# Kernel tuning notes

Hardware: AMD Instinct MI355X
Metric: run time of the kernel (lower is better)

Reference implementation:

```python
import jax, jax.numpy as jnp
import numpy as np

B, NLB, NPB, SDIM = 128, 32, 160, 256  # complexes, ligand atoms, pocket CAs, scalar dim


def _uniform(key, shape, fan_in):
    # kaiming_uniform_(a=sqrt(5)) -> U(-1/sqrt(fan_in), 1/sqrt(fan_in))
    bound = 1.0 / np.sqrt(fan_in)
    return jax.random.uniform(key, shape, jnp.float32, -bound, bound)


def setup_inputs() -> dict:
    key = jax.random.key(0)
    k1, k2, k3, k4, k5 = jax.random.split(key, 5)
    NL, NP = B * NLB, B * NPB
    # block-diagonal cross adjacency: every ligand atom paired with every pocket CA
    # of the same complex (same as (batch_ligand[:,None]==batch_pocket[None,:]).nonzero().T)
    l = np.repeat(np.arange(NL, dtype=np.int32), NPB)
    p = (np.arange(B, dtype=np.int32)[:, None, None] * NPB
         + np.zeros((1, NLB, 1), dtype=np.int32)
         + np.arange(NPB, dtype=np.int32)[None, None, :]).reshape(-1)
    return {
        "s_ligand": jax.random.normal(k1, (NL, SDIM), jnp.float32),
        "s_pocket": jax.random.normal(k2, (NP, SDIM), jnp.float32),
        "l": jnp.asarray(l),
        "p": jnp.asarray(p),
        "W1": _uniform(k3, (SDIM // 2, SDIM), SDIM),
        "b1": jnp.zeros((SDIM // 2,), jnp.float32),
        "W2": _uniform(k4, (SDIM // 4, SDIM // 2), SDIM // 2),
        "b2": jnp.zeros((SDIM // 4,), jnp.float32),
        "W3": _uniform(k5, (1, SDIM // 4), SDIM // 4),
        "b3": jnp.zeros((1,), jnp.float32),
    }


def reference(s_ligand, s_pocket, l, p, W1, b1, W2, b2, W3, b3):
    # gather cross-pair embeddings and sum: s[e] = s_ligand[l[e]] + s_pocket[p[e]]
    s = s_ligand[l] + s_pocket[p]                      # [E, sdim]
    h = jax.nn.silu(s @ W1.T + b1)                     # [E, sdim/2]
    h = jax.nn.silu(h @ W2.T + b2)                     # [E, sdim/4]
    out = jax.nn.relu(h @ W3.T + b3)                   # [E, 1]
    return out.squeeze(-1)                             # [E]
```

## Files before the change

kernel.cpp:

```cpp
#include <hip/hip_runtime.h>
#include <hip/hip_bf16.h>


#define B_CPLX   128
#define NLB      32
#define NPB      160
#define SDIM     256
#define H1DIM    128
#define NL_TOT   (B_CPLX * NLB)
#define NP_TOT   (B_CPLX * NPB)
#define NROWS    (NL_TOT + NP_TOT)
#define E_TOT    (B_CPLX * NLB * NPB)

#define W1_LDS_STRIDE 264
#define JT_CHUNK 16
#define ZP_STRIDE 132

#define EDGE_BLOCKS (B_CPLX * 10)

#define NEG_LOG2E -1.4426950408889634f
#define NEG_LN2   -0.69314718055994531f

typedef __bf16 bf16x8 __attribute__((ext_vector_type(8)));
typedef __bf16 bf16x2 __attribute__((ext_vector_type(2)));
typedef unsigned short ushortx8 __attribute__((ext_vector_type(8)));
typedef unsigned short ushortx4 __attribute__((ext_vector_type(4)));
typedef unsigned uintx4 __attribute__((ext_vector_type(4)));
typedef float f32x4 __attribute__((ext_vector_type(4)));
typedef float f32x2 __attribute__((ext_vector_type(2)));

#if __has_builtin(__builtin_amdgcn_exp2f)
#define EXP2F(x) __builtin_amdgcn_exp2f(x)
#else
#define EXP2F(x) exp2f(x)
#endif

__device__ __forceinline__ unsigned short f2bf(float f) {
    unsigned u = __builtin_bit_cast(unsigned, f);
    u += 0x7FFFu + ((u >> 16) & 1u);
    return (unsigned short)(u >> 16);
}

__device__ __forceinline__ unsigned perm_hi16u(unsigned u0, unsigned u1) {
    return __builtin_amdgcn_perm(u1, u0, 0x07060302u);
}

__device__ __forceinline__ unsigned pack2_rhu(float x0, float x1) {
    unsigned u0 = __builtin_bit_cast(unsigned, x0) + 0x8000u;
    unsigned u1 = __builtin_bit_cast(unsigned, x1) + 0x8000u;
    return perm_hi16u(u0, u1);
}

__device__ __forceinline__ bf16x8 pack8_rne(const float* x) {
    bf16x8 r;
#pragma unroll
    for (int j = 0; j < 4; ++j) {
        f32x2 p = {x[2 * j], x[2 * j + 1]};
        bf16x2 b = __builtin_convertvector(p, bf16x2);
        r[2 * j]     = b[0];
        r[2 * j + 1] = b[1];
    }
    return r;
}

__device__ __forceinline__ void pack_split(const float* x, bf16x8& hi, bf16x8& lo) {
    uintx4 h, l;
#pragma unroll
    for (int j = 0; j < 4; ++j) {
        float x0 = x[2 * j], x1 = x[2 * j + 1];
        unsigned u0 = __builtin_bit_cast(unsigned, x0);
        unsigned u1 = __builtin_bit_cast(unsigned, x1);
        h[j] = perm_hi16u(u0, u1);
        float hf0 = __builtin_bit_cast(float, u0 & 0xFFFF0000u);
        float hf1 = __builtin_bit_cast(float, u1 & 0xFFFF0000u);
        l[j] = pack2_rhu(x0 - hf0, x1 - hf1);
    }
    hi = __builtin_bit_cast(bf16x8, h);
    lo = __builtin_bit_cast(bf16x8, l);
}

__device__ __forceinline__ float silu_u(float t) {
    float e = EXP2F(t);
    float r = __builtin_amdgcn_rcpf(1.0f + e);
    return t * r;
}

__device__ __forceinline__ float rowsum16(float s) {
    int b;
    b = __builtin_bit_cast(int, s);
    b = __builtin_amdgcn_update_dpp(b, b, 0x121, 0xF, 0xF, false);
    s += __builtin_bit_cast(float, b);
    b = __builtin_bit_cast(int, s);
    b = __builtin_amdgcn_update_dpp(b, b, 0x122, 0xF, 0xF, false);
    s += __builtin_bit_cast(float, b);
    b = __builtin_bit_cast(int, s);
    b = __builtin_amdgcn_update_dpp(b, b, 0x124, 0xF, 0xF, false);
    s += __builtin_bit_cast(float, b);
    b = __builtin_bit_cast(int, s);
    b = __builtin_amdgcn_update_dpp(b, b, 0x128, 0xF, 0xF, false);
    s += __builtin_bit_cast(float, b);
    return s;
}

__global__ __launch_bounds__(256) void proj_kernel(
    const float* __restrict__ s_lig, const float* __restrict__ s_poc,
    const float* __restrict__ W1,    const float* __restrict__ b1,
    float* __restrict__ Z)
{
    __shared__ unsigned short w1s[64 * W1_LDS_STRIDE];

    const int tid  = threadIdx.x;
    const int tg   = blockIdx.x >> 1;
    const int half = blockIdx.x & 1;

    {
        const f32x4* w4 = (const f32x4*)(W1 + (size_t)half * 64 * SDIM);
#pragma unroll
        for (int r = 0; r < 2; ++r) {
            f32x4 t[8];
#pragma unroll
            for (int s = 0; s < 8; ++s) t[s] = w4[tid + (r * 8 + s) * 256];
#pragma unroll
            for (int s = 0; s < 8; ++s) {
                const int u = tid + (r * 8 + s) * 256;
                const int n = u >> 6;
                const int k4 = u & 63;
                ushortx4 us;
#pragma unroll
                for (int j = 0; j < 4; ++j) us[j] = f2bf(t[s][j]);
                *(ushortx4*)(&w1s[n * W1_LDS_STRIDE + k4 * 4]) = us;
            }
        }
    }
    __syncthreads();

    const int lane = tid & 63;
    const int widx = tid >> 6;
    const int c    = lane & 15;
    const int q    = lane >> 4;
    const int tile = tg * 4 + widx;
    const int row  = tile * 16 + c;

    const float* src = (row < NL_TOT) ? (s_lig + (size_t)row * SDIM)
                                      : (s_poc + (size_t)(row - NL_TOT) * SDIM);

    f32x4 acc[4];
#pragma unroll
    for (int nt = 0; nt < 4; ++nt) acc[nt] = (f32x4){0.f, 0.f, 0.f, 0.f};

#pragma unroll
    for (int ks = 0; ks < 8; ++ks) {
        const int k0 = ks * 32 + q * 8;
        f32x4 xa = *reinterpret_cast<const f32x4*>(src + k0);
        f32x4 xb = *reinterpret_cast<const f32x4*>(src + k0 + 4);
        float xv[8] = {xa[0], xa[1], xa[2], xa[3], xb[0], xb[1], xb[2], xb[3]};
        bf16x8 ahi, alo;
        pack_split(xv, ahi, alo);
        bf16x8 bfrag[4];
#pragma unroll
        for (int nt = 0; nt < 4; ++nt)
            bfrag[nt] = *reinterpret_cast<const bf16x8*>(
                &w1s[(nt * 16 + c) * W1_LDS_STRIDE + k0]);
#pragma unroll
        for (int nt = 0; nt < 4; ++nt)
            acc[nt] = __builtin_amdgcn_mfma_f32_16x16x32_bf16(ahi, bfrag[nt], acc[nt], 0, 0, 0);
#pragma unroll
        for (int nt = 0; nt < 4; ++nt)
            acc[nt] = __builtin_amdgcn_mfma_f32_16x16x32_bf16(alo, bfrag[nt], acc[nt], 0, 0, 0);
    }

    const int mb = tile * 16 + q * 4;
#pragma unroll
    for (int nt = 0; nt < 4; ++nt) {
        const int n = half * 64 + nt * 16 + c;
        const float bias = b1[n];
#pragma unroll
        for (int r = 0; r < 4; ++r) {
            const int m = mb + r;
            float v = acc[nt][r];
            if (m < NL_TOT) v += bias;
            Z[(size_t)m * H1DIM + n] = v;
        }
    }
}

__global__ __launch_bounds__(256) void edge_kernel(
    const float* __restrict__ Z,
    const float* __restrict__ W2, const float* __restrict__ b2,
    const float* __restrict__ W3, const float* __restrict__ b3,
    float* __restrict__ out)
{
    __shared__ float zp[JT_CHUNK * ZP_STRIDE];
    __shared__ float zl[NLB * H1DIM];
    __shared__ unsigned short w2s[16 * 64 * 8];

    const int tid = threadIdx.x;
    const int b   = blockIdx.x / 10;
    const int jt  = blockIdx.x - b * 10;

    {
#pragma unroll
        for (int s = 0; s < 4; ++s) {
            const int slot   = tid + s * 256;
            const int lane_s = slot & 63;
            const int chunk  = slot >> 6;
            const int nt     = chunk >> 2;
            const int ks     = chunk & 3;
            const int n      = nt * 16 + (lane_s & 15);
            const int k0     = ks * 32 + (lane_s >> 4) * 8;
            const float* wsrc = W2 + (size_t)n * H1DIM + k0;
            f32x4 wa = *(const f32x4*)wsrc;
            f32x4 wb = *(const f32x4*)(wsrc + 4);
            ushortx8 us;
#pragma unroll
            for (int j = 0; j < 4; ++j) {
                us[j]     = f2bf(wa[j]);
                us[4 + j] = f2bf(wb[j]);
            }
            *(ushortx8*)(&w2s[slot * 8]) = us;
        }
    }

    {
        const float* zpg = Z + (size_t)(NL_TOT + b * NPB + jt * JT_CHUNK) * H1DIM;
#pragma unroll
        for (int s = 0; s < 2; ++s) {
            const int u   = tid + s * 256;
            const int row = u >> 5;
            const int c4  = u & 31;
            f32x4 v = *(const f32x4*)(zpg + (size_t)row * H1DIM + c4 * 4);
            v *= NEG_LOG2E;
            *(f32x4*)(&zp[row * ZP_STRIDE + c4 * 4]) = v;
        }
    }

    {
        const float* zlg = Z + (size_t)(b * NLB) * H1DIM;
#pragma unroll
        for (int s = 0; s < 4; ++s) {
            const int u   = tid + s * 256;
            const int row = u >> 5;
            const int c4  = u & 31;
            f32x4 v = *(const f32x4*)(zlg + (size_t)row * H1DIM + c4 * 4);
            v *= NEG_LOG2E;
            *(f32x4*)(&zl[row * H1DIM + c4 * 4]) = v;
        }
    }

    const int lane = tid & 63;
    const int widx = tid >> 6;
    const int c    = lane & 15;
    const int q    = lane >> 4;

    float b2f[4], w3f[4];
#pragma unroll
    for (int nt = 0; nt < 4; ++nt) {
        b2f[nt] = b2[nt * 16 + c] * NEG_LOG2E;
        w3f[nt] = W3[nt * 16 + c] * NEG_LN2;
    }
    const float b3v = b3[0];

    __syncthreads();

    const float* prow = &zp[c * ZP_STRIDE];
    const unsigned short* wbase = &w2s[lane * 8];

#pragma unroll
    for (int h = 0; h < 2; ++h) {
        f32x4 acc[4][4];
#pragma unroll
        for (int a = 0; a < 4; ++a)
#pragma unroll
            for (int nt = 0; nt < 4; ++nt) {
                const float bb = b2f[nt];
                acc[a][nt] = (f32x4){bb, bb, bb, bb};
            }

        const float* lrow0 = &zl[(h * 16 + widx * 4) * H1DIM];

#pragma unroll
        for (int ks = 0; ks < 4; ++ks) {
            const int k0 = ks * 32 + q * 8;
            bf16x8 bfr[4];
#pragma unroll
            for (int nt = 0; nt < 4; ++nt)
                bfr[nt] = *(const bf16x8*)(wbase + (nt * 4 + ks) * 512);
            f32x4 pa = *(const f32x4*)(prow + k0);
            f32x4 pb = *(const f32x4*)(prow + k0 + 4);
#pragma unroll
            for (int a = 0; a < 4; ++a) {
                f32x4 la0 = *(const f32x4*)(lrow0 + a * H1DIM + k0);
                f32x4 la1 = *(const f32x4*)(lrow0 + a * H1DIM + k0 + 4);
                float hv[8];
#pragma unroll
                for (int j = 0; j < 4; ++j) {
                    hv[j]     = silu_u(pa[j] + la0[j]);
                    hv[4 + j] = silu_u(pb[j] + la1[j]);
                }
                bf16x8 af = pack8_rne(hv);
#pragma unroll
                for (int nt = 0; nt < 4; ++nt)
                    acc[a][nt] = __builtin_amdgcn_mfma_f32_16x16x32_bf16(af, bfr[nt], acc[a][nt], 0, 0, 0);
            }
        }

#pragma unroll
        for (int at = 0; at < 4; ++at) {
            const f32x4* A = acc[at];
            float s0 = 0.f, s1 = 0.f, s2 = 0.f, s3 = 0.f;
#pragma unroll
            for (int nt = 0; nt < 4; ++nt) {
                s0 += silu_u(A[nt][0]) * w3f[nt];
                s1 += silu_u(A[nt][1]) * w3f[nt];
                s2 += silu_u(A[nt][2]) * w3f[nt];
                s3 += silu_u(A[nt][3]) * w3f[nt];
            }
            s0 = rowsum16(s0);
            s1 = rowsum16(s1);
            s2 = rowsum16(s2);
            s3 = rowsum16(s3);
            if (c < 4) {
                float v = (c == 0) ? s0 : (c == 1) ? s1 : (c == 2) ? s2 : s3;
                const int e0 = (b * NLB + h * 16 + widx * 4 + at) * NPB + jt * JT_CHUNK;
                out[e0 + q * 4 + c] = fmaxf(v + b3v, 0.0f);
            }
        }
    }
}

extern "C" void kernel_launch(void* const* d_in, const int* in_sizes, int n_in,
                              void* d_out, int out_size, void* d_ws, size_t ws_size,
                              hipStream_t stream)
{
    const float* s_lig = (const float*)d_in[0];
    const float* s_poc = (const float*)d_in[1];
    const float* W1    = (const float*)d_in[4];
    const float* b1    = (const float*)d_in[5];
    const float* W2    = (const float*)d_in[6];
    const float* b2    = (const float*)d_in[7];
    const float* W3    = (const float*)d_in[8];
    const float* b3    = (const float*)d_in[9];

    float* Z = (float*)d_ws;

    hipLaunchKernelGGL(proj_kernel, dim3(NROWS / 16 / 4 * 2), dim3(256), 0, stream,
                       s_lig, s_poc, W1, b1, Z);
    hipLaunchKernelGGL(edge_kernel, dim3(EDGE_BLOCKS), dim3(256), 0, stream,
                       Z, W2, b2, W3, b3, (float*)d_out);
}
```

Before: 131.4 us.

## Prepack W2 in proj kernel, fold exp scaling into W1, swap MFMA operands

Block 0 of the projection kernel now converts W2 to bf16 fragment layout once and stores it in workspace, so edge blocks copy it directly instead of converting per block. The -log2(e) scale is folded into W1 and b1, which removes the per-element multiply when Z is staged in the edge kernel. The layer-2 MFMA operands are swapped so each lane holds four output channels for one edge, letting the W3 dot product finish with two cross-lane shuffles instead of four 16-lane DPP row sums. The cost is an extra workspace buffer and a small serial W2 conversion inside one proj block.

```diff
diff --git a/kernel.cpp b/kernel.cpp
--- a/kernel.cpp
+++ b/kernel.cpp
@@ -85,27 +85,11 @@
     return t * r;
 }
 
-__device__ __forceinline__ float rowsum16(float s) {
-    int b;
-    b = __builtin_bit_cast(int, s);
-    b = __builtin_amdgcn_update_dpp(b, b, 0x121, 0xF, 0xF, false);
-    s += __builtin_bit_cast(float, b);
-    b = __builtin_bit_cast(int, s);
-    b = __builtin_amdgcn_update_dpp(b, b, 0x122, 0xF, 0xF, false);
-    s += __builtin_bit_cast(float, b);
-    b = __builtin_bit_cast(int, s);
-    b = __builtin_amdgcn_update_dpp(b, b, 0x124, 0xF, 0xF, false);
-    s += __builtin_bit_cast(float, b);
-    b = __builtin_bit_cast(int, s);
-    b = __builtin_amdgcn_update_dpp(b, b, 0x128, 0xF, 0xF, false);
-    s += __builtin_bit_cast(float, b);
-    return s;
-}
-
 __global__ __launch_bounds__(256) void proj_kernel(
     const float* __restrict__ s_lig, const float* __restrict__ s_poc,
     const float* __restrict__ W1,    const float* __restrict__ b1,
-    float* __restrict__ Z)
+    const float* __restrict__ W2,
+    float* __restrict__ Z,           unsigned short* __restrict__ W2F)
 {
     __shared__ unsigned short w1s[64 * W1_LDS_STRIDE];
 
@@ -113,92 +97,7 @@
     const int tg   = blockIdx.x >> 1;
     const int half = blockIdx.x & 1;
 
-    {
-        const f32x4* w4 = (const f32x4*)(W1 + (size_t)half * 64 * SDIM);
-#pragma unroll
-        for (int r = 0; r < 2; ++r) {
-            f32x4 t[8];
-#pragma unroll
-            for (int s = 0; s < 8; ++s) t[s] = w4[tid + (r * 8 + s) * 256];
-#pragma unroll
-            for (int s = 0; s < 8; ++s) {
-                const int u = tid + (r * 8 + s) * 256;
-                const int n = u >> 6;
-                const int k4 = u & 63;
-                ushortx4 us;
-#pragma unroll
-                for (int j = 0; j < 4; ++j) us[j] = f2bf(t[s][j]);
-                *(ushortx4*)(&w1s[n * W1_LDS_STRIDE + k4 * 4]) = us;
-            }
-        }
-    }
-    __syncthreads();
-
-    const int lane = tid & 63;
-    const int widx = tid >> 6;
-    const int c    = lane & 15;
-    const int q    = lane >> 4;
-    const int tile = tg * 4 + widx;
-    const int row  = tile * 16 + c;
-
-    const float* src = (row < NL_TOT) ? (s_lig + (size_t)row * SDIM)
-                                      : (s_poc + (size_t)(row - NL_TOT) * SDIM);
-
-    f32x4 acc[4];
-#pragma unroll
-    for (int nt = 0; nt < 4; ++nt) acc[nt] = (f32x4){0.f, 0.f, 0.f, 0.f};
-
-#pragma unroll
-    for (int ks = 0; ks < 8; ++ks) {
-        const int k0 = ks * 32 + q * 8;
-        f32x4 xa = *reinterpret_cast<const f32x4*>(src + k0);
-        f32x4 xb = *reinterpret_cast<const f32x4*>(src + k0 + 4);
-        float xv[8] = {xa[0], xa[1], xa[2], xa[3], xb[0], xb[1], xb[2], xb[3]};
-        bf16x8 ahi, alo;
-        pack_split(xv, ahi, alo);
-        bf16x8 bfrag[4];
-#pragma unroll
-        for (int nt = 0; nt < 4; ++nt)
-            bfrag[nt] = *reinterpret_cast<const bf16x8*>(
-                &w1s[(nt * 16 + c) * W1_LDS_STRIDE + k0]);
-#pragma unroll
-        for (int nt = 0; nt < 4; ++nt)
-            acc[nt] = __builtin_amdgcn_mfma_f32_16x16x32_bf16(ahi, bfrag[nt], acc[nt], 0, 0, 0);
-#pragma unroll
-        for (int nt = 0; nt < 4; ++nt)
-            acc[nt] = __builtin_amdgcn_mfma_f32_16x16x32_bf16(alo, bfrag[nt], acc[nt], 0, 0, 0);
-    }
-
-    const int mb = tile * 16 + q * 4;
-#pragma unroll
-    for (int nt = 0; nt < 4; ++nt) {
-        const int n = half * 64 + nt * 16 + c;
-        const float bias = b1[n];
-#pragma unroll
-        for (int r = 0; r < 4; ++r) {
-            const int m = mb + r;
-            float v = acc[nt][r];
-            if (m < NL_TOT) v += bias;
-            Z[(size_t)m * H1DIM + n] = v;
-        }
-    }
-}
-
-__global__ __launch_bounds__(256) void edge_kernel(
-    const float* __restrict__ Z,
-    const float* __restrict__ W2, const float* __restrict__ b2,
-    const float* __restrict__ W3, const float* __restrict__ b3,
-    float* __restrict__ out)
-{
-    __shared__ float zp[JT_CHUNK * ZP_STRIDE];
-    __shared__ float zl[NLB * H1DIM];
-    __shared__ unsigned short w2s[16 * 64 * 8];
-
-    const int tid = threadIdx.x;
-    const int b   = blockIdx.x / 10;
-    const int jt  = blockIdx.x - b * 10;
-
-    {
+    if (blockIdx.x == 0) {
 #pragma unroll
         for (int s = 0; s < 4; ++s) {
             const int slot   = tid + s * 256;
@@ -217,7 +116,99 @@
                 us[j]     = f2bf(wa[j]);
                 us[4 + j] = f2bf(wb[j]);
             }
-            *(ushortx8*)(&w2s[slot * 8]) = us;
+            *(ushortx8*)(&W2F[slot * 8]) = us;
+        }
+    }
+
+    {
+        const f32x4* w4 = (const f32x4*)(W1 + (size_t)half * 64 * SDIM);
+#pragma unroll
+        for (int r = 0; r < 2; ++r) {
+            f32x4 t[8];
+#pragma unroll
+            for (int s = 0; s < 8; ++s) t[s] = w4[tid + (r * 8 + s) * 256];
+#pragma unroll
+            for (int s = 0; s < 8; ++s) {
+                const int u = tid + (r * 8 + s) * 256;
+                const int n = u >> 6;
+                const int k4 = u & 63;
+                ushortx4 us;
+#pragma unroll
+                for (int j = 0; j < 4; ++j) us[j] = f2bf(t[s][j] * NEG_LOG2E);
+                *(ushortx4*)(&w1s[n * W1_LDS_STRIDE + k4 * 4]) = us;
+            }
+        }
+    }
+    __syncthreads();
+
+    const int lane = tid & 63;
+    const int widx = tid >> 6;
+    const int c    = lane & 15;
+    const int q    = lane >> 4;
+    const int tile = tg * 4 + widx;
+    const int row  = tile * 16 + c;
+
+    const float* src = (row < NL_TOT) ? (s_lig + (size_t)row * SDIM)
+                                      : (s_poc + (size_t)(row - NL_TOT) * SDIM);
+
+    f32x4 acc[4];
+#pragma unroll
+    for (int nt = 0; nt < 4; ++nt) acc[nt] = (f32x4){0.f, 0.f, 0.f, 0.f};
+
+#pragma unroll
+    for (int ks = 0; ks < 8; ++ks) {
+        const int k0 = ks * 32 + q * 8;
+        f32x4 xa = *reinterpret_cast<const f32x4*>(src + k0);
+        f32x4 xb = *reinterpret_cast<const f32x4*>(src + k0 + 4);
+        float xv[8] = {xa[0], xa[1], xa[2], xa[3], xb[0], xb[1], xb[2], xb[3]};
+        bf16x8 ahi, alo;
+        pack_split(xv, ahi, alo);
+        bf16x8 bfrag[4];
+#pragma unroll
+        for (int nt = 0; nt < 4; ++nt)
+            bfrag[nt] = *reinterpret_cast<const bf16x8*>(
+                &w1s[(nt * 16 + c) * W1_LDS_STRIDE + k0]);
+#pragma unroll
+        for (int nt = 0; nt < 4; ++nt)
+            acc[nt] = __builtin_amdgcn_mfma_f32_16x16x32_bf16(ahi, bfrag[nt], acc[nt], 0, 0, 0);
+#pragma unroll
+        for (int nt = 0; nt < 4; ++nt)
+            acc[nt] = __builtin_amdgcn_mfma_f32_16x16x32_bf16(alo, bfrag[nt], acc[nt], 0, 0, 0);
+    }
+
+    const int mb = tile * 16 + q * 4;
+#pragma unroll
+    for (int nt = 0; nt < 4; ++nt) {
+        const int n = half * 64 + nt * 16 + c;
+        const float bias = b1[n] * NEG_LOG2E;
+#pragma unroll
+        for (int r = 0; r < 4; ++r) {
+            const int m = mb + r;
+            float v = acc[nt][r];
+            if (m < NL_TOT) v += bias;
+            Z[(size_t)m * H1DIM + n] = v;
+        }
+    }
+}
+
+__global__ __launch_bounds__(256) void edge_kernel(
+    const float* __restrict__ Z,  const unsigned short* __restrict__ W2F,
+    const float* __restrict__ b2, const float* __restrict__ W3,
+    const float* __restrict__ b3, float* __restrict__ out)
+{
+    __shared__ float zp[JT_CHUNK * ZP_STRIDE];
+    __shared__ float zl[NLB * H1DIM];
+    __shared__ unsigned short w2s[16 * 64 * 8];
+
+    const int tid = threadIdx.x;
+    const int b   = blockIdx.x / 10;
+    const int jt  = blockIdx.x - b * 10;
+
+    {
+#pragma unroll
+        for (int s = 0; s < 4; ++s) {
+            const int slot = tid + s * 256;
+            *(ushortx8*)(&w2s[slot * 8]) = *(const ushortx8*)(&W2F[slot * 8]);
         }
     }
 
@@ -228,9 +219,8 @@
             const int u   = tid + s * 256;
             const int row = u >> 5;
             const int c4  = u & 31;
-            f32x4 v = *(const f32x4*)(zpg + (size_t)row * H1DIM + c4 * 4);
-            v *= NEG_LOG2E;
-            *(f32x4*)(&zp[row * ZP_STRIDE + c4 * 4]) = v;
+            *(f32x4*)(&zp[row * ZP_STRIDE + c4 * 4]) =
+                *(const f32x4*)(zpg + (size_t)row * H1DIM + c4 * 4);
         }
     }
 
@@ -241,9 +231,8 @@
             const int u   = tid + s * 256;
             const int row = u >> 5;
             const int c4  = u & 31;
-            f32x4 v = *(const f32x4*)(zlg + (size_t)row * H1DIM + c4 * 4);
-            v *= NEG_LOG2E;
-            *(f32x4*)(&zl[row * H1DIM + c4 * 4]) = v;
+            *(f32x4*)(&zl[row * H1DIM + c4 * 4]) =
+                *(const f32x4*)(zlg + (size_t)row * H1DIM + c4 * 4);
         }
     }
 
@@ -252,11 +241,13 @@
     const int c    = lane & 15;
     const int q    = lane >> 4;
 
-    float b2f[4], w3f[4];
+    f32x4 b2v[4], w3v[4];
 #pragma unroll
     for (int nt = 0; nt < 4; ++nt) {
-        b2f[nt] = b2[nt * 16 + c] * NEG_LOG2E;
-        w3f[nt] = W3[nt * 16 + c] * NEG_LN2;
+        f32x4 bv = *(const f32x4*)(b2 + nt * 16 + q * 4);
+        f32x4 wv = *(const f32x4*)(W3 + nt * 16 + q * 4);
+        b2v[nt] = bv * NEG_LOG2E;
+        w3v[nt] = wv * NEG_LN2;
     }
     const float b3v = b3[0];
 
@@ -271,10 +262,7 @@
 #pragma unroll
         for (int a = 0; a < 4; ++a)
 #pragma unroll
-            for (int nt = 0; nt < 4; ++nt) {
-                const float bb = b2f[nt];
-                acc[a][nt] = (f32x4){bb, bb, bb, bb};
-            }
+            for (int nt = 0; nt < 4; ++nt) acc[a][nt] = b2v[nt];
 
         const float* lrow0 = &zl[(h * 16 + widx * 4) * H1DIM];
 
@@ -300,7 +288,7 @@
                 bf16x8 af = pack8_rne(hv);
 #pragma unroll
                 for (int nt = 0; nt < 4; ++nt)
-                    acc[a][nt] = __builtin_amdgcn_mfma_f32_16x16x32_bf16(af, bfr[nt], acc[a][nt], 0, 0, 0);
+                    acc[a][nt] = __builtin_amdgcn_mfma_f32_16x16x32_bf16(bfr[nt], af, acc[a][nt], 0, 0, 0);
             }
         }
 
@@ -310,19 +298,17 @@
             float s0 = 0.f, s1 = 0.f, s2 = 0.f, s3 = 0.f;
 #pragma unroll
             for (int nt = 0; nt < 4; ++nt) {
-                s0 += silu_u(A[nt][0]) * w3f[nt];
-                s1 += silu_u(A[nt][1]) * w3f[nt];
-                s2 += silu_u(A[nt][2]) * w3f[nt];
-                s3 += silu_u(A[nt][3]) * w3f[nt];
-            }
-            s0 = rowsum16(s0);
-            s1 = rowsum16(s1);
-            s2 = rowsum16(s2);
-            s3 = rowsum16(s3);
-            if (c < 4) {
-                float v = (c == 0) ? s0 : (c == 1) ? s1 : (c == 2) ? s2 : s3;
+                s0 += silu_u(A[nt][0]) * w3v[nt][0];
+                s1 += silu_u(A[nt][1]) * w3v[nt][1];
+                s2 += silu_u(A[nt][2]) * w3v[nt][2];
+                s3 += silu_u(A[nt][3]) * w3v[nt][3];
+            }
+            float v = (s0 + s1) + (s2 + s3);
+            v += __shfl_xor(v, 16);
+            v += __shfl_xor(v, 32);
+            if (lane < 16) {
                 const int e0 = (b * NLB + h * 16 + widx * 4 + at) * NPB + jt * JT_CHUNK;
-                out[e0 + q * 4 + c] = fmaxf(v + b3v, 0.0f);
+                out[e0 + lane] = fmaxf(v + b3v, 0.0f);
             }
         }
     }
@@ -342,9 +328,10 @@
     const float* b3    = (const float*)d_in[9];
 
     float* Z = (float*)d_ws;
+    unsigned short* W2F = (unsigned short*)(Z + (size_t)NROWS * H1DIM);
 
     hipLaunchKernelGGL(proj_kernel, dim3(NROWS / 16 / 4 * 2), dim3(256), 0, stream,
-                       s_lig, s_poc, W1, b1, Z);
+                       s_lig, s_poc, W1, b1, W2, Z, W2F);
     hipLaunchKernelGGL(edge_kernel, dim3(EDGE_BLOCKS), dim3(256), 0, stream,
-                       Z, W2, b2, W3, b3, (float*)d_out);
-}
+                       Z, W2F, b2, W3, b3, (float*)d_out);
+}
```

Result: no change. 130.3 us (-0.8%).
